# Kernel tuning notes

Measured on AMD Instinct MI355X. Metric: run time of the kernel, lower is better.

The kernel has to match this reference:

```python
import jax, jax.numpy as jnp
import numpy as np

RH, RW = 40, 64          # render image height/width
SAM_HW = 64              # SAM ViT-H feature map spatial size
FEAT_DIM = 17            # voxel_feature_dim
GAUSSIAN_SEM_WEIGHT = 1.0


def nearest_resize(x, oh, ow):
    # torch F.interpolate mode='nearest': idx = floor(out_idx * in/out)
    ih, iw = x.shape[-2], x.shape[-1]
    ri = jnp.floor(jnp.arange(oh) * (ih / oh)).astype(jnp.int32)
    ci = jnp.floor(jnp.arange(ow) * (iw / ow)).astype(jnp.int32)
    return x[..., ri, :][..., ci]


def bilinear_resize(x, oh, ow):
    # torch bilinear, align_corners=False (half-pixel centers)
    ih, iw = x.shape[-2], x.shape[-1]
    def axis(isz, osz):
        src = (jnp.arange(osz, dtype=x.dtype) + 0.5) * (isz / osz) - 0.5
        i0 = jnp.clip(jnp.floor(src), 0, isz - 1).astype(jnp.int32)
        i1 = jnp.clip(i0 + 1, 0, isz - 1)
        w = jnp.clip(src - i0.astype(x.dtype), 0.0, 1.0)
        return i0, i1, w
    r0, r1, wr = axis(ih, oh)
    c0, c1, wc = axis(iw, ow)
    xr = x[..., r0, :] * (1 - wr)[:, None] + x[..., r1, :] * wr[:, None]
    return xr[..., c0] * (1 - wc) + xr[..., c1] * wc


def quat_to_rot(q):  # q: [N,4] normalized (w,x,y,z)
    w, x, y, z = q[:, 0], q[:, 1], q[:, 2], q[:, 3]
    R = jnp.stack([
        1 - 2 * (y * y + z * z), 2 * (x * y - w * z), 2 * (x * z + w * y),
        2 * (x * y + w * z), 1 - 2 * (x * x + z * z), 2 * (y * z - w * x),
        2 * (x * z - w * y), 2 * (y * z + w * x), 1 - 2 * (x * x + y * y)], -1)
    return R.reshape(-1, 3, 3)


def sam_proj(x, W1, b1, g1, be1, W2, b2, g2, be2, W3, b3):
    # Linear -> LayerNorm -> LeakyReLU (x2) -> Linear, all on last dim
    def ln(h, g, b):
        mu = h.mean(-1, keepdims=True)
        var = ((h - mu) ** 2).mean(-1, keepdims=True)
        return (h - mu) / jnp.sqrt(var + 1e-5) * g + b
    h = jax.nn.leaky_relu(ln(x @ W1.T + b1, g1, be1), 0.01)
    h = jax.nn.leaky_relu(ln(h @ W2.T + b2, g2, be2), 0.01)
    return h @ W3.T + b3


def render_feature_map(xyz, feats, opac, scal, quat, vm, intr):
    # Differentiable EWA Gaussian-splat feature rasterizer (3DGS-style math).
    N = xyz.shape[0]
    Rw, t = vm[:3, :3], vm[:3, 3]
    cam = xyz @ Rw.T + t                      # [N,3] camera coords
    x, y, z = cam[:, 0], cam[:, 1], cam[:, 2]
    fx, fy, cx, cy = intr[0], intr[1], intr[2], intr[3]
    zc = jnp.maximum(z, 1e-3)
    u = fx * x / zc + cx
    v = fy * y / zc + cy
    # 3D covariance Sigma = R S S^T R^T, transformed to camera then projected
    Rq = quat_to_rot(quat)
    M = Rq * scal[:, None, :]
    cov3 = M @ jnp.swapaxes(M, 1, 2)          # [N,3,3]
    covw = jnp.einsum('ij,njk,lk->nil', Rw, cov3, Rw)
    inv_z = 1.0 / zc
    zero = jnp.zeros_like(z)
    J = jnp.stack([
        jnp.stack([fx * inv_z, zero, -fx * x * inv_z ** 2], -1),
        jnp.stack([zero, fy * inv_z, -fy * y * inv_z ** 2], -1)], 1)  # [N,2,3]
    cov2 = jnp.einsum('nij,njk,nlk->nil', J, covw, J)
    a = cov2[:, 0, 0] + 0.3
    bq = cov2[:, 0, 1]
    cc = cov2[:, 1, 1] + 0.3
    det = a * cc - bq * bq
    A, Bc, Cc = cc / det, -bq / det, a / det   # conic (inverse 2D cov)
    xx, yy = jnp.meshgrid(jnp.arange(RW, dtype=xyz.dtype), jnp.arange(RH, dtype=xyz.dtype))
    px, py = xx.reshape(-1), yy.reshape(-1)    # [P]
    dx = u[:, None] - px[None, :]              # [N,P]
    dy = v[:, None] - py[None, :]
    power = -0.5 * (A[:, None] * dx * dx + Cc[:, None] * dy * dy) - Bc[:, None] * dx * dy
    alpha = jnp.minimum(0.99, opac * jnp.exp(jnp.minimum(power, 0.0)))
    alpha = alpha * (z > 0.2).astype(alpha.dtype)[:, None]
    # depth-sorted alpha compositing
    order = jnp.argsort(z)
    a_s = alpha[order]                         # [N,P]
    f_s = feats[order]                         # [N,C]
    T = jnp.concatenate([jnp.ones((1, a_s.shape[1]), a_s.dtype),
                         jnp.cumprod(1.0 - a_s, axis=0)[:-1]], axis=0)
    out = jnp.einsum('np,nc->cp', a_s * T, f_s)  # white_background=False -> bg 0
    return out.reshape(FEAT_DIM, RH, RW)


def _forward(voxel_feats, opacity, sam_embd, sam_features, sam_masks, viewmat,
             intrins, pc_xyz, scales, rots, W1, b1, g1, be1, W2, b2, g2, be2, W3, b3):
    B, C = viewmat.shape[0], viewmat.shape[1]
    scal = jnp.exp(scales)
    quat = rots / jnp.linalg.norm(rots, axis=-1, keepdims=True)
    proj = lambda x: sam_proj(x, W1, b1, g1, be1, W2, b2, g2, be2, W3, b3)
    loss_batch = 0.0
    for b in range(B):
        vf = voxel_feats[b].reshape(-1, FEAT_DIM)
        op = opacity[b].reshape(-1, 1)
        loss_c = 0.0
        for c in range(C):
            fmap = render_feature_map(pc_xyz, vf, op, scal, quat, viewmat[b, c], intrins[b, c])
            # use_sam: L1 between rendered map and projected SAM embedding
            se = nearest_resize(sam_embd[b, c], RH, RW)          # [256,RH,RW]
            sed = proj(se.transpose(1, 2, 0))                    # [RH,RW,17]
            loss_c = loss_c + jnp.abs(fmap.transpose(1, 2, 0) - sed).mean()
            # SAM mask contrastive loss
            sf = sam_features[b, c]                              # [256,64,64]
            ldf = proj(sf.reshape(256, -1).T).T.reshape(FEAT_DIM, SAM_HW, SAM_HW)
            masks = sam_masks[b, c]                              # [M,200,200]
            lsm = nearest_resize(masks, SAM_HW, SAM_HW)          # [M,64,64]
            proto = jnp.einsum('mhw,chw->mc', lsm, ldf)
            proto = proto / jnp.maximum(lsm.sum((1, 2)), 1e-6)[:, None]
            prob = jax.nn.sigmoid(jnp.einsum('mc,chw->mhw', proto, fmap))
            frm = bilinear_resize(masks, RH, RW)
            frm = jnp.where(frm <= 0.5, 0.0, frm)
            bce = frm * jnp.log(prob + 1e-8) + (1 - frm) * jnp.log(1 - prob + 1e-8)
            loss_c = loss_c - bce.mean()
        loss_batch = loss_batch + loss_c / C
    return loss_batch / B * GAUSSIAN_SEM_WEIGHT


def setup_inputs() -> dict:
    key = jax.random.key(0)
    ks = jax.random.split(key, 10)
    vs = 2.0
    gx1 = np.arange(-40.0, 40.0 + vs - 0.1, vs)
    gx = (gx1[:40] + gx1[1:41]) / 2
    gy = gx.copy()
    gz1 = np.arange(-2.4, 13.6 + vs - 0.1, vs)
    gz = (gz1[:8] + gz1[1:9]) / 2
    X, Y, Z = np.meshgrid(gx, gy, gz, indexing='ij')
    pc_xyz = np.stack([X, Y, Z], -1).reshape(-1, 3).astype(np.float32)
    N = pc_xyz.shape[0]  # 12800
    # regular grid: 3-NN mean squared dist = vs^2 -> scales = log(sqrt(vs^2))
    scales = np.full((N, 3), np.log(vs), np.float32)
    rots = np.zeros((N, 4), np.float32); rots[:, 0] = 1.0
    vm = np.zeros((1, 2, 4, 4), np.float32)
    vm[0, :, 0, 0] = vm[0, :, 1, 1] = vm[0, :, 2, 2] = vm[0, :, 3, 3] = 1.0
    vm[0, 0, :3, 3] = [0.0, 0.0, 60.0]
    vm[0, 1, :3, 3] = [2.0, -1.0, 62.0]
    intr = np.tile(np.array([32.0, 20.0, 32.0, 20.0], np.float32), (1, 2, 1))
    inp = {
        'voxel_feats': jax.random.normal(ks[0], (1, N, 17), jnp.float32) * 0.5,
        'opacity': jax.random.uniform(ks[1], (1, N, 1), jnp.float32) * 0.1,
        'sam_embd': jax.random.normal(ks[2], (1, 2, 256, 64, 64), jnp.float32),
        'sam_features': jax.random.normal(ks[3], (1, 2, 256, 64, 64), jnp.float32),
        'sam_masks': (jax.random.uniform(ks[4], (1, 2, 16, 200, 200)) < 0.3).astype(jnp.float32),
        'viewmat': jnp.asarray(vm), 'intrins': jnp.asarray(intr),
        'pc_xyz': jnp.asarray(pc_xyz), 'scales': jnp.asarray(scales), 'rots': jnp.asarray(rots),
        'W1': jax.random.normal(ks[5], (64, 256), jnp.float32) * 0.05,
        'b1': jnp.zeros((64,), jnp.float32),
        'g1': jnp.ones((64,), jnp.float32), 'be1': jnp.zeros((64,), jnp.float32),
        'W2': jax.random.normal(ks[6], (64, 64), jnp.float32) * 0.1,
        'b2': jnp.zeros((64,), jnp.float32),
        'g2': jnp.ones((64,), jnp.float32), 'be2': jnp.zeros((64,), jnp.float32),
        'W3': jax.random.normal(ks[7], (17, 64), jnp.float32) * 0.1,
        'b3': jnp.zeros((17,), jnp.float32),
    }
    return inp


def reference(voxel_feats, opacity, sam_embd, sam_features, sam_masks, viewmat,
              intrins, pc_xyz, scales, rots, W1, b1, g1, be1, W2, b2, g2, be2, W3, b3):
    return _forward(voxel_feats, opacity, sam_embd, sam_features, sam_masks, viewmat,
                    intrins, pc_xyz, scales, rots, W1, b1, g1, be1, W2, b2, g2, be2, W3, b3)
```

## Files before the change

kernel.cpp:

```cpp
#include <hip/hip_runtime.h>
#include <math.h>

#define NPTS   12800
#define P_PIX  2560
#define NC     32
#define CHUNK  400
#define RANK_CHUNK 800
#define RT     4
#define MLP_PITCH 264

typedef short short8 __attribute__((ext_vector_type(8)));
typedef float f32x4 __attribute__((ext_vector_type(4)));
typedef float f32x2 __attribute__((ext_vector_type(2)));

__device__ __forceinline__ unsigned short f2bf(float f) {
    unsigned int u = __float_as_uint(f);
    u += 0x7fffu + ((u >> 16) & 1u);
    return (unsigned short)(u >> 16);
}

__global__ __launch_bounds__(256) void prep_kernel(
    const float* __restrict__ xyz, const float* __restrict__ scales,
    const float* __restrict__ rots, const float* __restrict__ opacity,
    const float* __restrict__ viewmat, const float* __restrict__ intrins,
    unsigned long long* __restrict__ keys,
    float* __restrict__ pu, float* __restrict__ pv, float* __restrict__ prad,
    float* __restrict__ phA, float* __restrict__ phC, float* __restrict__ pnB,
    float* __restrict__ pop, int* __restrict__ rnk, float* __restrict__ out, int N) {
    int cam = blockIdx.y;
    int i = blockIdx.x * 256 + threadIdx.x;
    if (i >= N) return;
    int idx = cam * N + i;
    rnk[idx] = 0;
    if (idx == 0) out[0] = 0.0f;
    const float* vm = viewmat + cam * 16;
    const float* it = intrins + cam * 4;
    float fx = it[0], fy = it[1], cx = it[2], cy = it[3];
    float R00 = vm[0], R01 = vm[1], R02 = vm[2], t0 = vm[3];
    float R10 = vm[4], R11 = vm[5], R12 = vm[6], t1 = vm[7];
    float R20 = vm[8], R21 = vm[9], R22 = vm[10], t2 = vm[11];
    float X = xyz[i * 3], Y = xyz[i * 3 + 1], Z = xyz[i * 3 + 2];
    float x = R00 * X + R01 * Y + R02 * Z + t0;
    float y = R10 * X + R11 * Y + R12 * Z + t1;
    float z = R20 * X + R21 * Y + R22 * Z + t2;
    float zc = fmaxf(z, 0.001f);
    float iz = 1.0f / zc;
    float u = fx * x * iz + cx;
    float v = fy * y * iz + cy;
    float qw = rots[i * 4], qx = rots[i * 4 + 1], qy = rots[i * 4 + 2], qz = rots[i * 4 + 3];
    float qn = 1.0f / sqrtf(qw * qw + qx * qx + qy * qy + qz * qz);
    qw *= qn; qx *= qn; qy *= qn; qz *= qn;
    float s0 = expf(scales[i * 3]), s1 = expf(scales[i * 3 + 1]), s2 = expf(scales[i * 3 + 2]);
    float Rq[3][3] = {
        {1 - 2 * (qy * qy + qz * qz), 2 * (qx * qy - qw * qz), 2 * (qx * qz + qw * qy)},
        {2 * (qx * qy + qw * qz), 1 - 2 * (qx * qx + qz * qz), 2 * (qy * qz - qw * qx)},
        {2 * (qx * qz - qw * qy), 2 * (qy * qz + qw * qx), 1 - 2 * (qx * qx + qy * qy)}};
    float M[3][3];
    #pragma unroll
    for (int r = 0; r < 3; ++r) { M[r][0] = Rq[r][0] * s0; M[r][1] = Rq[r][1] * s1; M[r][2] = Rq[r][2] * s2; }
    float c3[3][3];
    #pragma unroll
    for (int a = 0; a < 3; ++a)
        #pragma unroll
        for (int b = 0; b < 3; ++b)
            c3[a][b] = M[a][0] * M[b][0] + M[a][1] * M[b][1] + M[a][2] * M[b][2];
    float Rw[3][3] = {{R00, R01, R02}, {R10, R11, R12}, {R20, R21, R22}};
    float Wt[3][3];
    #pragma unroll
    for (int a = 0; a < 3; ++a)
        #pragma unroll
        for (int b = 0; b < 3; ++b)
            Wt[a][b] = Rw[a][0] * c3[0][b] + Rw[a][1] * c3[1][b] + Rw[a][2] * c3[2][b];
    float cw[3][3];
    #pragma unroll
    for (int a = 0; a < 3; ++a)
        #pragma unroll
        for (int b = 0; b < 3; ++b)
            cw[a][b] = Wt[a][0] * Rw[b][0] + Wt[a][1] * Rw[b][1] + Wt[a][2] * Rw[b][2];
    float j00 = fx * iz, j02 = -fx * x * iz * iz;
    float j11 = fy * iz, j12 = -fy * y * iz * iz;
    float c00 = j00 * j00 * cw[0][0] + 2.0f * j00 * j02 * cw[0][2] + j02 * j02 * cw[2][2];
    float c01 = j00 * j11 * cw[0][1] + j00 * j12 * cw[0][2] + j02 * j11 * cw[2][1] + j02 * j12 * cw[2][2];
    float c11 = j11 * j11 * cw[1][1] + 2.0f * j11 * j12 * cw[1][2] + j12 * j12 * cw[2][2];
    float a = c00 + 0.3f, bq = c01, cc = c11 + 0.3f;
    float det = a * cc - bq * bq;
    float A = cc / det, Bc = -bq / det, Cc = a / det;
    float lmin = 0.5f * ((A + Cc) - sqrtf((A - Cc) * (A - Cc) + 4.0f * Bc * Bc));
    lmin = fmaxf(lmin, 1e-20f);
    float opv = (z > 0.2f) ? opacity[i] : 0.0f;
    float rad = -1.0f;
    if (opv > 0.0f) {
        float tcut = logf(opv) + 18.42f;
        if (tcut > 0.0f) rad = sqrtf(2.0f * tcut / lmin);
    }
    pu[idx] = u; pv[idx] = v; prad[idx] = rad;
    phA[idx] = -0.5f * A; phC[idx] = -0.5f * Cc; pnB[idx] = -Bc;
    pop[idx] = opv;
    unsigned int zb = __float_as_uint(z);
    zb = (zb & 0x80000000u) ? ~zb : (zb | 0x80000000u);
    keys[idx] = ((unsigned long long)zb << 32) | (unsigned int)i;
}

__global__ __launch_bounds__(256) void rank_kernel(const unsigned long long* __restrict__ keys,
                                                   int* __restrict__ rnk, int N) {
    __shared__ unsigned long long sk[RANK_CHUNK];
    int cam = blockIdx.z;
    const unsigned long long* K = keys + (size_t)cam * N;
    int jbase = blockIdx.y * RANK_CHUNK;
    int jcnt = min(RANK_CHUNK, N - jbase);
    for (int t = threadIdx.x; t < jcnt; t += 256) sk[t] = K[jbase + t];
    __syncthreads();
    int i0 = blockIdx.x * (256 * RT) + threadIdx.x;
    unsigned long long ki[RT];
    int cnt[RT];
    #pragma unroll
    for (int t = 0; t < RT; ++t) {
        int i = i0 + t * 256;
        ki[t] = (i < N) ? K[i] : 0xFFFFFFFFFFFFFFFFull;
        cnt[t] = 0;
    }
    #pragma unroll 4
    for (int j = 0; j < jcnt; ++j) {
        unsigned long long kj = sk[j];
        #pragma unroll
        for (int t = 0; t < RT; ++t) cnt[t] += (kj < ki[t]) ? 1 : 0;
    }
    #pragma unroll
    for (int t = 0; t < RT; ++t) {
        int i = i0 + t * 256;
        if (i < N && cnt[t]) atomicAdd(rnk + (size_t)cam * N + i, cnt[t]);
    }
}

__global__ __launch_bounds__(256) void scatter_kernel(
    const int* __restrict__ rnk,
    const float* __restrict__ pu, const float* __restrict__ pv, const float* __restrict__ prad,
    const float* __restrict__ phA, const float* __restrict__ phC, const float* __restrict__ pnB,
    const float* __restrict__ pop,
    const float* __restrict__ feats, float* __restrict__ rec, float2* __restrict__ vr, int N) {
    int cam = blockIdx.y;
    int i = blockIdx.x * 256 + threadIdx.x;
    if (i >= N) return;
    int idx = cam * N + i;
    int r = rnk[idx];
    float* d = rec + ((size_t)cam * N + r) * 24;
    d[0] = pu[idx]; d[1] = pv[idx]; d[2] = pop[idx]; d[3] = phA[idx];
    d[4] = phC[idx]; d[5] = pnB[idx];
    const float* f = feats + (size_t)i * 17;
    #pragma unroll
    for (int c = 0; c < 17; ++c) d[6 + c] = f[c];
    d[23] = 0.0f;
    vr[(size_t)cam * N + r] = make_float2(pv[idx], prad[idx]);
}

__global__ __launch_bounds__(256) void build_kernel(const float2* __restrict__ vr,
                                                    unsigned short* __restrict__ lists,
                                                    int* __restrict__ cnts, int N) {
    int gid = blockIdx.x * 4 + (threadIdx.x >> 6);
    int lane = threadIdx.x & 63;
    int cam = gid / (NC * 40);
    int rem = gid - cam * (NC * 40);
    int ch = rem / 40, row = rem - ch * 40;
    const float2* V = vr + (size_t)cam * N + ch * CHUNK;
    unsigned short* L = lists + (size_t)gid * CHUNK;
    float py = (float)row;
    int cnt = 0;
    for (int g = 0; g < CHUNK; g += 64) {
        int n = g + lane;
        bool pass = false;
        if (n < CHUNK) {
            float2 t = V[n];
            pass = fabsf(t.x - py) <= t.y + 0.01f;
        }
        unsigned long long mask = __ballot(pass);
        int pre = __popcll(mask & ((1ull << lane) - 1ull));
        if (pass) L[cnt + pre] = (unsigned short)n;
        cnt += __popcll(mask);
    }
    if (lane == 0) cnts[gid] = cnt;
}

__global__ __launch_bounds__(256) void splat_kernel(const float* __restrict__ rec,
                                                    const unsigned short* __restrict__ lists,
                                                    const int* __restrict__ cnts,
                                                    float* __restrict__ part, int N) {
    __shared__ __align__(16) float4 sRec[CHUNK * 6];
    __shared__ unsigned short sList[4 * CHUNK];
    __shared__ int sCnt[4];
    int cam = blockIdx.z, ch = blockIdx.y, pg = blockIdx.x;
    int tid = threadIdx.x, lane = tid & 63, wv = tid >> 6;
    const float4* src = (const float4*)(rec + ((size_t)cam * N + ch * CHUNK) * 24);
    for (int t = tid; t < CHUNK * 6; t += 256) sRec[t] = src[t];
    int lid0 = (cam * NC + ch) * 40 + pg * 4;
    const unsigned int* Lb = (const unsigned int*)(lists + (size_t)lid0 * CHUNK);
    unsigned int* sL = (unsigned int*)sList;
    for (int t = tid; t < 2 * CHUNK; t += 256) sL[t] = Lb[t];
    if (tid < 4) sCnt[tid] = cnts[lid0 + tid];
    __syncthreads();
    int row = pg * 4 + wv;
    int cnt = sCnt[wv];
    float px = (float)lane, py = (float)row;
    float T = 1.0f;
    f32x2 acc[9];
    #pragma unroll
    for (int j = 0; j < 9; ++j) acc[j] = (f32x2){0.f, 0.f};
    const unsigned short* myL = sList + wv * CHUNK;
    for (int i = 0; i < cnt; ++i) {
        int n = myL[i];
        const float4* rp = sRec + n * 6;
        float4 q0 = rp[0];
        float4 q1 = rp[1];
        float dx = q0.x - px, dy = q0.y - py;
        float t1 = (q1.y * dx) * dy;
        t1 = fmaf(q1.x * dy, dy, t1);
        float power = fminf(fmaf(q0.w * dx, dx, t1), 0.0f);
        float alpha = fminf(0.99f, q0.z * __expf(power));
        float w = alpha * T;
        f32x2 w2 = (f32x2){w, w};
        float4 q2 = rp[2], q3 = rp[3], q4 = rp[4], q5 = rp[5];
        acc[0] += w2 * (f32x2){q1.z, q1.w};
        acc[1] += w2 * (f32x2){q2.x, q2.y};
        acc[2] += w2 * (f32x2){q2.z, q2.w};
        acc[3] += w2 * (f32x2){q3.x, q3.y};
        acc[4] += w2 * (f32x2){q3.z, q3.w};
        acc[5] += w2 * (f32x2){q4.x, q4.y};
        acc[6] += w2 * (f32x2){q4.z, q4.w};
        acc[7] += w2 * (f32x2){q5.x, q5.y};
        acc[8] += w2 * (f32x2){q5.z, q5.w};
        T *= (1.0f - alpha);
    }
    int p0 = row * 64 + lane;
    size_t base = ((size_t)(cam * NC + ch) * 18) * P_PIX;
    part[base + p0] = T;
    #pragma unroll
    for (int j = 0; j < 8; ++j) {
        part[base + (size_t)(1 + 2 * j) * P_PIX + p0] = acc[j][0];
        part[base + (size_t)(2 + 2 * j) * P_PIX + p0] = acc[j][1];
    }
    part[base + (size_t)17 * P_PIX + p0] = acc[8][0];
}

__global__ __launch_bounds__(256) void combine_kernel(const float* __restrict__ part,
                                                      float* __restrict__ fmap) {
    int idx = blockIdx.x * 256 + threadIdx.x;
    if (idx >= 2 * 17 * P_PIX) return;
    int p = idx % P_PIX;
    int rem = idx / P_PIX;
    int c = rem % 17;
    int cam = rem / 17;
    float acc = 0.0f, Tp = 1.0f;
    #pragma unroll 8
    for (int k = 0; k < NC; ++k) {
        size_t base = ((size_t)(cam * NC + k) * 18) * P_PIX + p;
        float Tk = part[base];
        float S  = part[base + (size_t)(1 + c) * P_PIX];
        acc = fmaf(Tp, S, acc);
        Tp *= Tk;
    }
    fmap[((size_t)cam * 17 + c) * P_PIX + p] = acc;
}

__global__ __launch_bounds__(256, 2) void mlp_kernel(
    const float* __restrict__ embd, const float* __restrict__ sfeat,
    const float* __restrict__ W1, const float* __restrict__ b1,
    const float* __restrict__ g1, const float* __restrict__ be1,
    const float* __restrict__ W2, const float* __restrict__ b2,
    const float* __restrict__ g2, const float* __restrict__ be2,
    const float* __restrict__ W3, const float* __restrict__ b3,
    float* __restrict__ sed, float* __restrict__ ldf) {
    __shared__ __align__(16) unsigned short smem[2 * 64 * MLP_PITCH];
    unsigned short* sX = smem;
    unsigned short* sW = smem + 64 * MLP_PITCH;
    int tid = threadIdx.x, lane = tid & 63, wv = tid >> 6;
    int m = lane & 15, kq = lane >> 4, q4 = kq * 4;
    int tile = blockIdx.x;
    const float* xbase;
    if (tile < 80) {
        int cam = tile / 40; int r = tile - cam * 40;
        int ri = (r * 8) / 5;
        xbase = embd + (size_t)cam * 256 * 4096 + ri * 64;
    } else {
        int tt = tile - 80; int cam = tt >> 6;
        xbase = sfeat + (size_t)cam * 256 * 4096 + (tt & 63) * 64;
    }
    const float4* xf4 = (const float4*)xbase;
    for (int idx = tid; idx < 4096; idx += 256) {
        int k = idx >> 4, q = idx & 15;
        float4 xv = xf4[(size_t)k * 1024 + q];
        int r = q * 4;
        sX[(r + 0) * MLP_PITCH + k] = f2bf(xv.x);
        sX[(r + 1) * MLP_PITCH + k] = f2bf(xv.y);
        sX[(r + 2) * MLP_PITCH + k] = f2bf(xv.z);
        sX[(r + 3) * MLP_PITCH + k] = f2bf(xv.w);
    }
    const float4* wf4 = (const float4*)W1;
    for (int idx = tid; idx < 4096; idx += 256) {
        float4 wvv = wf4[idx];
        int n = idx >> 6, kk = (idx & 63) * 4;
        uint2 pk;
        pk.x = (unsigned int)f2bf(wvv.x) | ((unsigned int)f2bf(wvv.y) << 16);
        pk.y = (unsigned int)f2bf(wvv.z) | ((unsigned int)f2bf(wvv.w) << 16);
        *(uint2*)&sW[n * MLP_PITCH + kk] = pk;
    }
    float b1v[4], g1v[4], be1v[4], b2v[4], g2v[4], be2v[4];
    #pragma unroll
    for (int nt = 0; nt < 4; ++nt) {
        int c = nt * 16 + m;
        b1v[nt] = b1[c]; g1v[nt] = g1[c]; be1v[nt] = be1[c];
        b2v[nt] = b2[c]; g2v[nt] = g2[c]; be2v[nt] = be2[c];
    }
    __syncthreads();
    f32x4 acc[4];
    #pragma unroll
    for (int nt = 0; nt < 4; ++nt) acc[nt] = (f32x4){0.f, 0.f, 0.f, 0.f};
    const unsigned short* aptr = sX + (wv * 16 + m) * MLP_PITCH + kq * 8;
    const unsigned short* bptr = sW + m * MLP_PITCH + kq * 8;
    #pragma unroll
    for (int ks = 0; ks < 8; ++ks) {
        short8 af = *(const short8*)(aptr + ks * 32);
        #pragma unroll
        for (int nt = 0; nt < 4; ++nt) {
            short8 bf = *(const short8*)(bptr + nt * 16 * MLP_PITCH + ks * 32);
            acc[nt] = __builtin_amdgcn_mfma_f32_16x16x32_bf16(af, bf, acc[nt], 0, 0, 0);
        }
    }
    __syncthreads();
    unsigned short* hbuf  = smem + wv * 16 * 72;
    unsigned short* hbuf2 = smem + (4 + wv) * 16 * 72;
    unsigned short* W2b = sW;
    unsigned short* W3b = sW + 64 * 72;
    for (int i = tid; i < 4096; i += 256)
        W2b[(i >> 6) * 72 + (i & 63)] = f2bf(W2[i]);
    for (int i = tid; i < 2048; i += 256) {
        int n = i >> 6, k = i & 63;
        W3b[n * 72 + k] = (n < 17) ? f2bf(W3[n * 64 + k]) : 0;
    }
    #pragma unroll
    for (int rg = 0; rg < 4; ++rg) {
        float h0 = acc[0][rg] + b1v[0], h1 = acc[1][rg] + b1v[1];
        float h2 = acc[2][rg] + b1v[2], h3 = acc[3][rg] + b1v[3];
        float s = (h0 + h1) + (h2 + h3);
        s += __shfl_xor(s, 1); s += __shfl_xor(s, 2);
        s += __shfl_xor(s, 4); s += __shfl_xor(s, 8);
        float mu = s * (1.0f / 64.0f);
        float d0 = h0 - mu, d1 = h1 - mu, d2 = h2 - mu, d3 = h3 - mu;
        float vs = (d0 * d0 + d1 * d1) + (d2 * d2 + d3 * d3);
        vs += __shfl_xor(vs, 1); vs += __shfl_xor(vs, 2);
        vs += __shfl_xor(vs, 4); vs += __shfl_xor(vs, 8);
        float rstd = 1.0f / sqrtf(vs * (1.0f / 64.0f) + 1e-5f);
        float hn0 = d0 * rstd * g1v[0] + be1v[0]; hn0 = fmaxf(hn0, 0.01f * hn0);
        float hn1 = d1 * rstd * g1v[1] + be1v[1]; hn1 = fmaxf(hn1, 0.01f * hn1);
        float hn2 = d2 * rstd * g1v[2] + be1v[2]; hn2 = fmaxf(hn2, 0.01f * hn2);
        float hn3 = d3 * rstd * g1v[3] + be1v[3]; hn3 = fmaxf(hn3, 0.01f * hn3);
        int rr = (q4 + rg) * 72 + m;
        hbuf[rr] = f2bf(hn0); hbuf[rr + 16] = f2bf(hn1);
        hbuf[rr + 32] = f2bf(hn2); hbuf[rr + 48] = f2bf(hn3);
    }
    __syncthreads();
    f32x4 acc2[4];
    #pragma unroll
    for (int nt = 0; nt < 4; ++nt) acc2[nt] = (f32x4){0.f, 0.f, 0.f, 0.f};
    const unsigned short* a2p = hbuf + m * 72 + kq * 8;
    #pragma unroll
    for (int ks = 0; ks < 2; ++ks) {
        short8 af = *(const short8*)(a2p + ks * 32);
        #pragma unroll
        for (int nt = 0; nt < 4; ++nt) {
            short8 bf = *(const short8*)(W2b + (nt * 16 + m) * 72 + kq * 8 + ks * 32);
            acc2[nt] = __builtin_amdgcn_mfma_f32_16x16x32_bf16(af, bf, acc2[nt], 0, 0, 0);
        }
    }
    #pragma unroll
    for (int rg = 0; rg < 4; ++rg) {
        float h0 = acc2[0][rg] + b2v[0], h1 = acc2[1][rg] + b2v[1];
        float h2 = acc2[2][rg] + b2v[2], h3 = acc2[3][rg] + b2v[3];
        float s = (h0 + h1) + (h2 + h3);
        s += __shfl_xor(s, 1); s += __shfl_xor(s, 2);
        s += __shfl_xor(s, 4); s += __shfl_xor(s, 8);
        float mu = s * (1.0f / 64.0f);
        float d0 = h0 - mu, d1 = h1 - mu, d2 = h2 - mu, d3 = h3 - mu;
        float vs = (d0 * d0 + d1 * d1) + (d2 * d2 + d3 * d3);
        vs += __shfl_xor(vs, 1); vs += __shfl_xor(vs, 2);
        vs += __shfl_xor(vs, 4); vs += __shfl_xor(vs, 8);
        float rstd = 1.0f / sqrtf(vs * (1.0f / 64.0f) + 1e-5f);
        float hn0 = d0 * rstd * g2v[0] + be2v[0]; hn0 = fmaxf(hn0, 0.01f * hn0);
        float hn1 = d1 * rstd * g2v[1] + be2v[1]; hn1 = fmaxf(hn1, 0.01f * hn1);
        float hn2 = d2 * rstd * g2v[2] + be2v[2]; hn2 = fmaxf(hn2, 0.01f * hn2);
        float hn3 = d3 * rstd * g2v[3] + be2v[3]; hn3 = fmaxf(hn3, 0.01f * hn3);
        int rr = (q4 + rg) * 72 + m;
        hbuf2[rr] = f2bf(hn0); hbuf2[rr + 16] = f2bf(hn1);
        hbuf2[rr + 32] = f2bf(hn2); hbuf2[rr + 48] = f2bf(hn3);
    }
    f32x4 acc3[2];
    acc3[0] = (f32x4){0.f, 0.f, 0.f, 0.f};
    acc3[1] = (f32x4){0.f, 0.f, 0.f, 0.f};
    const unsigned short* a3p = hbuf2 + m * 72 + kq * 8;
    #pragma unroll
    for (int ks = 0; ks < 2; ++ks) {
        short8 af = *(const short8*)(a3p + ks * 32);
        #pragma unroll
        for (int nt = 0; nt < 2; ++nt) {
            short8 bf = *(const short8*)(W3b + (nt * 16 + m) * 72 + kq * 8 + ks * 32);
            acc3[nt] = __builtin_amdgcn_mfma_f32_16x16x32_bf16(af, bf, acc3[nt], 0, 0, 0);
        }
    }
    #pragma unroll
    for (int nt = 0; nt < 2; ++nt) {
        int c = nt * 16 + m;
        if (c < 17) {
            float b3v = b3[c];
            #pragma unroll
            for (int rg = 0; rg < 4; ++rg) {
                int row = tile * 64 + wv * 16 + q4 + rg;
                float val = acc3[nt][rg] + b3v;
                if (row < 5120) {
                    int cam = row / 2560; int p = row - cam * 2560;
                    sed[((size_t)cam * 2560 + p) * 17 + c] = val;
                } else {
                    int rr = row - 5120; int cam = rr >> 12; int t = rr & 4095;
                    ldf[((size_t)cam * 17 + c) * 4096 + t] = val;
                }
            }
        }
    }
}

__global__ __launch_bounds__(256) void proto_kernel(const float* __restrict__ masks,
                                                    const float* __restrict__ ldf,
                                                    float* __restrict__ proto) {
    int cam = blockIdx.y, m = blockIdx.x;
    const float* M = masks + ((size_t)cam * 16 + m) * 40000;
    float acc[18];
    #pragma unroll
    for (int j = 0; j < 18; ++j) acc[j] = 0.0f;
    for (int t = threadIdx.x; t < 4096; t += 256) {
        int h = t >> 6, w = t & 63;
        int rh = (h * 25) >> 3, rw = (w * 25) >> 3;
        float lv = M[rh * 200 + rw];
        if (lv != 0.0f) {
            acc[17] += lv;
            const float* L = ldf + (size_t)cam * 17 * 4096 + t;
            #pragma unroll
            for (int c = 0; c < 17; ++c) acc[c] = fmaf(lv, L[(size_t)c * 4096], acc[c]);
        }
    }
    __shared__ float red[4][18];
    int lane = threadIdx.x & 63, wv = threadIdx.x >> 6;
    #pragma unroll
    for (int j = 0; j < 18; ++j) {
        float v = acc[j];
        #pragma unroll
        for (int o = 32; o; o >>= 1) v += __shfl_xor(v, o);
        if (lane == 0) red[wv][j] = v;
    }
    __syncthreads();
    if (threadIdx.x < 17) {
        float sacc = red[0][threadIdx.x] + red[1][threadIdx.x] + red[2][threadIdx.x] + red[3][threadIdx.x];
        float ms = red[0][17] + red[1][17] + red[2][17] + red[3][17];
        proto[((size_t)cam * 16 + m) * 17 + threadIdx.x] = sacc / fmaxf(ms, 1e-6f);
    }
}

__device__ __forceinline__ void block_atomic_add(float v, float* target) {
    #pragma unroll
    for (int o = 32; o; o >>= 1) v += __shfl_xor(v, o);
    __shared__ float sred[4];
    int lane = threadIdx.x & 63, wv = threadIdx.x >> 6;
    if (lane == 0) sred[wv] = v;
    __syncthreads();
    if (threadIdx.x == 0) atomicAdd(target, sred[0] + sred[1] + sred[2] + sred[3]);
}

__global__ __launch_bounds__(256) void bce_kernel(const float* __restrict__ masks,
                                                  const float* __restrict__ proto,
                                                  const float* __restrict__ fmap,
                                                  const float* __restrict__ sed,
                                                  float* __restrict__ out) {
    int idx = blockIdx.x * 256 + threadIdx.x;
    int p = idx % P_PIX;
    int rem = idx / P_PIX;
    int m = rem & 15, cam = rem >> 4;
    const float* pr = proto + ((size_t)cam * 16 + m) * 17;
    float f[17];
    #pragma unroll
    for (int c = 0; c < 17; ++c) f[c] = fmap[((size_t)cam * 17 + c) * P_PIX + p];
    float sdot = 0;
    #pragma unroll
    for (int c = 0; c < 17; ++c) sdot = fmaf(pr[c], f[c], sdot);
    float prob = 1.0f / (1.0f + __expf(-sdot));
    int px = p & 63, py = p >> 6;
    float src_r = (py + 0.5f) * 5.0f - 0.5f;
    float src_c = (px + 0.5f) * 3.125f - 0.5f;
    int r0 = (int)fminf(fmaxf(floorf(src_r), 0.0f), 199.0f);
    int r1 = min(r0 + 1, 199);
    float wr = fminf(fmaxf(src_r - (float)r0, 0.0f), 1.0f);
    int c0 = (int)fminf(fmaxf(floorf(src_c), 0.0f), 199.0f);
    int c1 = min(c0 + 1, 199);
    float wc = fminf(fmaxf(src_c - (float)c0, 0.0f), 1.0f);
    const float* M = masks + ((size_t)cam * 16 + m) * 40000;
    float v00 = M[r0 * 200 + c0], v01 = M[r0 * 200 + c1];
    float v10 = M[r1 * 200 + c0], v11 = M[r1 * 200 + c1];
    float xr0 = v00 * (1.0f - wr) + v10 * wr;
    float xr1 = v01 * (1.0f - wr) + v11 * wr;
    float frm = xr0 * (1.0f - wc) + xr1 * wc;
    frm = (frm <= 0.5f) ? 0.0f : frm;
    float bce = frm * __logf(prob + 1e-8f) + (1.0f - frm) * __logf(1.0f - prob + 1e-8f);
    float val = bce * (-1.0f / (16.0f * 2560.0f * 2.0f));
    if (m == 0) {
        float ssum = 0.0f;
        const float* sp = sed + ((size_t)cam * P_PIX + p) * 17;
        #pragma unroll
        for (int c = 0; c < 17; ++c) ssum += fabsf(f[c] - sp[c]);
        val += ssum * (1.0f / (43520.0f * 2.0f));
    }
    block_atomic_add(val, out);
}

extern "C" void kernel_launch(void* const* d_in, const int* in_sizes, int n_in,
                              void* d_out, int out_size, void* d_ws, size_t ws_size,
                              hipStream_t stream) {
    const float* voxel_feats = (const float*)d_in[0];
    const float* opacity     = (const float*)d_in[1];
    const float* sam_embd    = (const float*)d_in[2];
    const float* sam_features= (const float*)d_in[3];
    const float* sam_masks   = (const float*)d_in[4];
    const float* viewmat     = (const float*)d_in[5];
    const float* intrins     = (const float*)d_in[6];
    const float* pc_xyz      = (const float*)d_in[7];
    const float* scales      = (const float*)d_in[8];
    const float* rots        = (const float*)d_in[9];
    const float* W1 = (const float*)d_in[10], *b1 = (const float*)d_in[11];
    const float* g1 = (const float*)d_in[12], *be1 = (const float*)d_in[13];
    const float* W2 = (const float*)d_in[14], *b2 = (const float*)d_in[15];
    const float* g2 = (const float*)d_in[16], *be2 = (const float*)d_in[17];
    const float* W3 = (const float*)d_in[18], *b3 = (const float*)d_in[19];
    float* out = (float*)d_out;
    const int N = in_sizes[7] / 3;

    char* w = (char*)d_ws;
    size_t off = 0;
    auto alloc = [&](size_t bytes) -> void* {
        off = (off + 255) & ~(size_t)255;
        void* p = w + off; off += bytes; return p;
    };
    int* rnk  = (int*)alloc((size_t)2 * N * sizeof(int));
    unsigned long long* keys = (unsigned long long*)alloc((size_t)2 * N * 8);
    float* params = (float*)alloc((size_t)7 * 2 * N * 4);
    float* pu  = params,           *pv  = params + 2 * N,  *prad = params + 4 * N;
    float* phA = params + 6 * N,   *phC = params + 8 * N,  *pnB  = params + 10 * N;
    float* pop = params + 12 * N;
    float* rec   = (float*)alloc((size_t)2 * N * 24 * 4);
    float2* vr   = (float2*)alloc((size_t)2 * N * 8);
    float* part  = (float*)alloc((size_t)2 * NC * 18 * P_PIX * 4);
    float* fmap  = (float*)alloc((size_t)2 * 17 * P_PIX * 4);
    float* sed   = (float*)alloc((size_t)2 * P_PIX * 17 * 4);
    float* ldf   = (float*)alloc((size_t)2 * 17 * 4096 * 4);
    float* proto = (float*)alloc((size_t)2 * 16 * 17 * 4);
    unsigned short* lists = (unsigned short*)alloc((size_t)2 * NC * 40 * CHUNK * 2);
    int* cnts = (int*)alloc((size_t)2 * NC * 40 * sizeof(int));

    dim3 gprep((N + 255) / 256, 2);
    prep_kernel<<<gprep, 256, 0, stream>>>(pc_xyz, scales, rots, opacity, viewmat, intrins,
                                           keys, pu, pv, prad, phA, phC, pnB, pop, rnk, out, N);
    dim3 grank((N + 256 * RT - 1) / (256 * RT), (N + RANK_CHUNK - 1) / RANK_CHUNK, 2);
    rank_kernel<<<grank, 256, 0, stream>>>(keys, rnk, N);
    scatter_kernel<<<gprep, 256, 0, stream>>>(rnk, pu, pv, prad, phA, phC, pnB, pop,
                                              voxel_feats, rec, vr, N);
    build_kernel<<<2 * NC * 40 / 4, 256, 0, stream>>>(vr, lists, cnts, N);
    dim3 gsplat(10, NC, 2);
    splat_kernel<<<gsplat, 256, 0, stream>>>(rec, lists, cnts, part, N);
    mlp_kernel<<<208, 256, 0, stream>>>(sam_embd, sam_features, W1, b1, g1, be1,
                                        W2, b2, g2, be2, W3, b3, sed, ldf);
    combine_kernel<<<(2 * 17 * P_PIX + 255) / 256, 256, 0, stream>>>(part, fmap);
    dim3 gproto(16, 2);
    proto_kernel<<<gproto, 256, 0, stream>>>(sam_masks, ldf, proto);
    bce_kernel<<<(2 * 16 * P_PIX) / 256, 256, 0, stream>>>(sam_masks, proto, fmap, sed, out);
}
```

Measured before the change: 233.5 us.

## Pack splat records to fp16, process four rows per wave, halve chunk size

```diff
diff --git a/kernel.cpp b/kernel.cpp
--- a/kernel.cpp
+++ b/kernel.cpp
@@ -3,8 +3,8 @@
 
 #define NPTS   12800
 #define P_PIX  2560
-#define NC     32
-#define CHUNK  400
+#define NC     64
+#define CHUNK  200
 #define RANK_CHUNK 800
 #define RT     4
 #define MLP_PITCH 264
@@ -17,6 +17,16 @@
     unsigned int u = __float_as_uint(f);
     u += 0x7fffu + ((u >> 16) & 1u);
     return (unsigned short)(u >> 16);
+}
+
+__device__ __forceinline__ float pack2h(float a, float b) {
+    union { float f; _Float16 h[2]; } c;
+    c.h[0] = (_Float16)a; c.h[1] = (_Float16)b;
+    return c.f;
+}
+__device__ __forceinline__ float2 unpk2h(float w) {
+    union { float f; _Float16 h[2]; } c; c.f = w;
+    return make_float2((float)c.h[0], (float)c.h[1]);
 }
 
 __global__ __launch_bounds__(256) void prep_kernel(
@@ -143,104 +153,135 @@
     if (i >= N) return;
     int idx = cam * N + i;
     int r = rnk[idx];
-    float* d = rec + ((size_t)cam * N + r) * 24;
-    d[0] = pu[idx]; d[1] = pv[idx]; d[2] = pop[idx]; d[3] = phA[idx];
-    d[4] = phC[idx]; d[5] = pnB[idx];
+    float* d = rec + ((size_t)cam * N + r) * 16;
+    d[0] = pu[idx]; d[1] = pv[idx];
+    d[2] = pack2h(phA[idx], phC[idx]);
+    d[3] = pack2h(pnB[idx], pop[idx]);
     const float* f = feats + (size_t)i * 17;
     #pragma unroll
-    for (int c = 0; c < 17; ++c) d[6 + c] = f[c];
-    d[23] = 0.0f;
+    for (int j = 0; j < 8; ++j) d[4 + j] = pack2h(f[2 * j], f[2 * j + 1]);
+    d[12] = pack2h(f[16], 0.0f);
+    d[13] = 0.0f; d[14] = 0.0f; d[15] = 0.0f;
     vr[(size_t)cam * N + r] = make_float2(pv[idx], prad[idx]);
 }
 
 __global__ __launch_bounds__(256) void build_kernel(const float2* __restrict__ vr,
-                                                    unsigned short* __restrict__ lists,
+                                                    unsigned char* __restrict__ lists,
                                                     int* __restrict__ cnts, int N) {
     int gid = blockIdx.x * 4 + (threadIdx.x >> 6);
     int lane = threadIdx.x & 63;
-    int cam = gid / (NC * 40);
-    int rem = gid - cam * (NC * 40);
-    int ch = rem / 40, row = rem - ch * 40;
+    int cam = gid / (NC * 10);
+    int rem = gid - cam * (NC * 10);
+    int ch = rem / 10, rg = rem - ch * 10;
     const float2* V = vr + (size_t)cam * N + ch * CHUNK;
-    unsigned short* L = lists + (size_t)gid * CHUNK;
-    float py = (float)row;
+    unsigned char* L = lists + (size_t)gid * CHUNK;
+    float cy = (float)(rg * 4) + 1.5f;
     int cnt = 0;
     for (int g = 0; g < CHUNK; g += 64) {
         int n = g + lane;
         bool pass = false;
         if (n < CHUNK) {
             float2 t = V[n];
-            pass = fabsf(t.x - py) <= t.y + 0.01f;
+            pass = fabsf(t.x - cy) <= t.y + 1.51f;
         }
         unsigned long long mask = __ballot(pass);
         int pre = __popcll(mask & ((1ull << lane) - 1ull));
-        if (pass) L[cnt + pre] = (unsigned short)n;
+        if (pass) L[cnt + pre] = (unsigned char)n;
         cnt += __popcll(mask);
     }
     if (lane == 0) cnts[gid] = cnt;
 }
 
-__global__ __launch_bounds__(256) void splat_kernel(const float* __restrict__ rec,
-                                                    const unsigned short* __restrict__ lists,
+__global__ __launch_bounds__(128) void splat_kernel(const float* __restrict__ rec,
+                                                    const unsigned char* __restrict__ lists,
                                                     const int* __restrict__ cnts,
-                                                    float* __restrict__ part, int N) {
-    __shared__ __align__(16) float4 sRec[CHUNK * 6];
-    __shared__ unsigned short sList[4 * CHUNK];
-    __shared__ int sCnt[4];
+                                                    float* __restrict__ partT,
+                                                    unsigned short* __restrict__ partS, int N) {
+    __shared__ __align__(16) float4 sRec[CHUNK * 4];
+    __shared__ unsigned char sList[2 * CHUNK];
+    __shared__ int sCnt[2];
     int cam = blockIdx.z, ch = blockIdx.y, pg = blockIdx.x;
     int tid = threadIdx.x, lane = tid & 63, wv = tid >> 6;
-    const float4* src = (const float4*)(rec + ((size_t)cam * N + ch * CHUNK) * 24);
-    for (int t = tid; t < CHUNK * 6; t += 256) sRec[t] = src[t];
-    int lid0 = (cam * NC + ch) * 40 + pg * 4;
+    const float4* src = (const float4*)(rec + ((size_t)cam * N + ch * CHUNK) * 16);
+    for (int t = tid; t < CHUNK * 4; t += 128) sRec[t] = src[t];
+    int lid0 = (cam * NC + ch) * 10 + pg * 2;
     const unsigned int* Lb = (const unsigned int*)(lists + (size_t)lid0 * CHUNK);
     unsigned int* sL = (unsigned int*)sList;
-    for (int t = tid; t < 2 * CHUNK; t += 256) sL[t] = Lb[t];
-    if (tid < 4) sCnt[tid] = cnts[lid0 + tid];
+    for (int t = tid; t < 2 * CHUNK / 4; t += 128) sL[t] = Lb[t];
+    if (tid < 2) sCnt[tid] = cnts[lid0 + tid];
     __syncthreads();
-    int row = pg * 4 + wv;
+    int r0 = pg * 8 + wv * 4;
     int cnt = sCnt[wv];
-    float px = (float)lane, py = (float)row;
-    float T = 1.0f;
-    f32x2 acc[9];
-    #pragma unroll
-    for (int j = 0; j < 9; ++j) acc[j] = (f32x2){0.f, 0.f};
-    const unsigned short* myL = sList + wv * CHUNK;
+    float px = (float)lane, py0 = (float)r0;
+    float T0 = 1.0f, T1 = 1.0f, T2 = 1.0f, T3 = 1.0f;
+    f32x2 accA[17], accB[17];
+    #pragma unroll
+    for (int c = 0; c < 17; ++c) { accA[c] = (f32x2){0.f, 0.f}; accB[c] = (f32x2){0.f, 0.f}; }
+    const unsigned char* myL = sList + wv * CHUNK;
+    const float* sRf = (const float*)sRec;
     for (int i = 0; i < cnt; ++i) {
         int n = myL[i];
-        const float4* rp = sRec + n * 6;
+        const float4* rp = sRec + n * 4;
         float4 q0 = rp[0];
-        float4 q1 = rp[1];
-        float dx = q0.x - px, dy = q0.y - py;
-        float t1 = (q1.y * dx) * dy;
-        t1 = fmaf(q1.x * dy, dy, t1);
-        float power = fminf(fmaf(q0.w * dx, dx, t1), 0.0f);
-        float alpha = fminf(0.99f, q0.z * __expf(power));
-        float w = alpha * T;
-        f32x2 w2 = (f32x2){w, w};
-        float4 q2 = rp[2], q3 = rp[3], q4 = rp[4], q5 = rp[5];
-        acc[0] += w2 * (f32x2){q1.z, q1.w};
-        acc[1] += w2 * (f32x2){q2.x, q2.y};
-        acc[2] += w2 * (f32x2){q2.z, q2.w};
-        acc[3] += w2 * (f32x2){q3.x, q3.y};
-        acc[4] += w2 * (f32x2){q3.z, q3.w};
-        acc[5] += w2 * (f32x2){q4.x, q4.y};
-        acc[6] += w2 * (f32x2){q4.z, q4.w};
-        acc[7] += w2 * (f32x2){q5.x, q5.y};
-        acc[8] += w2 * (f32x2){q5.z, q5.w};
-        T *= (1.0f - alpha);
-    }
-    int p0 = row * 64 + lane;
-    size_t base = ((size_t)(cam * NC + ch) * 18) * P_PIX;
-    part[base + p0] = T;
-    #pragma unroll
-    for (int j = 0; j < 8; ++j) {
-        part[base + (size_t)(1 + 2 * j) * P_PIX + p0] = acc[j][0];
-        part[base + (size_t)(2 + 2 * j) * P_PIX + p0] = acc[j][1];
-    }
-    part[base + (size_t)17 * P_PIX + p0] = acc[8][0];
-}
-
-__global__ __launch_bounds__(256) void combine_kernel(const float* __restrict__ part,
+        float2 g0 = unpk2h(q0.z);
+        float2 g1 = unpk2h(q0.w);
+        float dx = q0.x - px;
+        float dy0 = q0.y - py0, dy1 = dy0 - 1.0f, dy2 = dy0 - 2.0f, dy3 = dy0 - 3.0f;
+        float hAdx = g0.x * dx;
+        float p0 = fmaf(g0.y * dy0, dy0, dx * fmaf(g1.x, dy0, hAdx));
+        float p1 = fmaf(g0.y * dy1, dy1, dx * fmaf(g1.x, dy1, hAdx));
+        float p2 = fmaf(g0.y * dy2, dy2, dx * fmaf(g1.x, dy2, hAdx));
+        float p3 = fmaf(g0.y * dy3, dy3, dx * fmaf(g1.x, dy3, hAdx));
+        float a0 = fminf(0.99f, g1.y * __expf(fminf(p0, 0.0f)));
+        float a1 = fminf(0.99f, g1.y * __expf(fminf(p1, 0.0f)));
+        float a2 = fminf(0.99f, g1.y * __expf(fminf(p2, 0.0f)));
+        float a3 = fminf(0.99f, g1.y * __expf(fminf(p3, 0.0f)));
+        f32x2 wA = (f32x2){a0 * T0, a1 * T1};
+        f32x2 wB = (f32x2){a2 * T2, a3 * T3};
+        T0 = fmaf(-T0, a0, T0); T1 = fmaf(-T1, a1, T1);
+        T2 = fmaf(-T2, a2, T2); T3 = fmaf(-T3, a3, T3);
+        float4 q1 = rp[1], q2 = rp[2];
+        float q3x = sRf[n * 16 + 12];
+        float2 f01 = unpk2h(q1.x), f23 = unpk2h(q1.y), f45 = unpk2h(q1.z), f67 = unpk2h(q1.w);
+        float2 f89 = unpk2h(q2.x), fab = unpk2h(q2.y), fcd = unpk2h(q2.z), fef = unpk2h(q2.w);
+        float2 fg_ = unpk2h(q3x);
+        accA[0]  += wA * f01.x;  accB[0]  += wB * f01.x;
+        accA[1]  += wA * f01.y;  accB[1]  += wB * f01.y;
+        accA[2]  += wA * f23.x;  accB[2]  += wB * f23.x;
+        accA[3]  += wA * f23.y;  accB[3]  += wB * f23.y;
+        accA[4]  += wA * f45.x;  accB[4]  += wB * f45.x;
+        accA[5]  += wA * f45.y;  accB[5]  += wB * f45.y;
+        accA[6]  += wA * f67.x;  accB[6]  += wB * f67.x;
+        accA[7]  += wA * f67.y;  accB[7]  += wB * f67.y;
+        accA[8]  += wA * f89.x;  accB[8]  += wB * f89.x;
+        accA[9]  += wA * f89.y;  accB[9]  += wB * f89.y;
+        accA[10] += wA * fab.x;  accB[10] += wB * fab.x;
+        accA[11] += wA * fab.y;  accB[11] += wB * fab.y;
+        accA[12] += wA * fcd.x;  accB[12] += wB * fcd.x;
+        accA[13] += wA * fcd.y;  accB[13] += wB * fcd.y;
+        accA[14] += wA * fef.x;  accB[14] += wB * fef.x;
+        accA[15] += wA * fef.y;  accB[15] += wB * fef.y;
+        accA[16] += wA * fg_.x;  accB[16] += wB * fg_.x;
+    }
+    size_t cbase = (size_t)(cam * NC + ch);
+    size_t p0i = (size_t)r0 * 64 + lane;
+    partT[cbase * P_PIX + p0i]       = T0;
+    partT[cbase * P_PIX + p0i + 64]  = T1;
+    partT[cbase * P_PIX + p0i + 128] = T2;
+    partT[cbase * P_PIX + p0i + 192] = T3;
+    _Float16* pS = (_Float16*)partS;
+    #pragma unroll
+    for (int c = 0; c < 17; ++c) {
+        size_t b = (cbase * 17 + c) * P_PIX + p0i;
+        pS[b]       = (_Float16)accA[c][0];
+        pS[b + 64]  = (_Float16)accA[c][1];
+        pS[b + 128] = (_Float16)accB[c][0];
+        pS[b + 192] = (_Float16)accB[c][1];
+    }
+}
+
+__global__ __launch_bounds__(256) void combine_kernel(const float* __restrict__ partT,
+                                                      const unsigned short* __restrict__ partS,
                                                       float* __restrict__ fmap) {
     int idx = blockIdx.x * 256 + threadIdx.x;
     if (idx >= 2 * 17 * P_PIX) return;
@@ -248,12 +289,13 @@
     int rem = idx / P_PIX;
     int c = rem % 17;
     int cam = rem / 17;
+    const _Float16* pS = (const _Float16*)partS;
     float acc = 0.0f, Tp = 1.0f;
     #pragma unroll 8
     for (int k = 0; k < NC; ++k) {
-        size_t base = ((size_t)(cam * NC + k) * 18) * P_PIX + p;
-        float Tk = part[base];
-        float S  = part[base + (size_t)(1 + c) * P_PIX];
+        size_t cb = (size_t)(cam * NC + k);
+        float Tk = partT[cb * P_PIX + p];
+        float S = (float)pS[(cb * 17 + c) * P_PIX + p];
         acc = fmaf(Tp, S, acc);
         Tp *= Tk;
     }
@@ -549,15 +591,16 @@
     float* pu  = params,           *pv  = params + 2 * N,  *prad = params + 4 * N;
     float* phA = params + 6 * N,   *phC = params + 8 * N,  *pnB  = params + 10 * N;
     float* pop = params + 12 * N;
-    float* rec   = (float*)alloc((size_t)2 * N * 24 * 4);
+    float* rec   = (float*)alloc((size_t)2 * N * 16 * 4);
     float2* vr   = (float2*)alloc((size_t)2 * N * 8);
-    float* part  = (float*)alloc((size_t)2 * NC * 18 * P_PIX * 4);
+    float* partT = (float*)alloc((size_t)2 * NC * P_PIX * 4);
+    unsigned short* partS = (unsigned short*)alloc((size_t)2 * NC * 17 * P_PIX * 2);
     float* fmap  = (float*)alloc((size_t)2 * 17 * P_PIX * 4);
     float* sed   = (float*)alloc((size_t)2 * P_PIX * 17 * 4);
     float* ldf   = (float*)alloc((size_t)2 * 17 * 4096 * 4);
     float* proto = (float*)alloc((size_t)2 * 16 * 17 * 4);
-    unsigned short* lists = (unsigned short*)alloc((size_t)2 * NC * 40 * CHUNK * 2);
-    int* cnts = (int*)alloc((size_t)2 * NC * 40 * sizeof(int));
+    unsigned char* lists = (unsigned char*)alloc((size_t)2 * NC * 10 * CHUNK);
+    int* cnts = (int*)alloc((size_t)2 * NC * 10 * sizeof(int));
 
     dim3 gprep((N + 255) / 256, 2);
     prep_kernel<<<gprep, 256, 0, stream>>>(pc_xyz, scales, rots, opacity, viewmat, intrins,
@@ -566,12 +609,12 @@
     rank_kernel<<<grank, 256, 0, stream>>>(keys, rnk, N);
     scatter_kernel<<<gprep, 256, 0, stream>>>(rnk, pu, pv, prad, phA, phC, pnB, pop,
                                               voxel_feats, rec, vr, N);
-    build_kernel<<<2 * NC * 40 / 4, 256, 0, stream>>>(vr, lists, cnts, N);
-    dim3 gsplat(10, NC, 2);
-    splat_kernel<<<gsplat, 256, 0, stream>>>(rec, lists, cnts, part, N);
+    build_kernel<<<2 * NC * 10 / 4, 256, 0, stream>>>(vr, lists, cnts, N);
+    dim3 gsplat(5, NC, 2);
+    splat_kernel<<<gsplat, 128, 0, stream>>>(rec, lists, cnts, partT, partS, N);
     mlp_kernel<<<208, 256, 0, stream>>>(sam_embd, sam_features, W1, b1, g1, be1,
                                         W2, b2, g2, be2, W3, b3, sed, ldf);
-    combine_kernel<<<(2 * 17 * P_PIX + 255) / 256, 256, 0, stream>>>(part, fmap);
+    combine_kernel<<<(2 * 17 * P_PIX + 255) / 256, 256, 0, stream>>>(partT, partS, fmap);
     dim3 gproto(16, 2);
     proto_kernel<<<gproto, 256, 0, stream>>>(sam_masks, ldf, proto);
     bce_kernel<<<(2 * 16 * P_PIX) / 256, 256, 0, stream>>>(sam_masks, proto, fmap, sed, out);
```

New measurement: 266.3 us. 14.1% more time.
